# Optimization experiments

Measured on AMD Instinct MI355X. Metric: run time of the kernel, lower is better.

The kernel has to match this reference:

```python
import jax, jax.numpy as jnp
import numpy as np

NEG_INF = -9e15  # mask value used by the original module
LEAKY_SLOPE = 0.2


def setup_inputs() -> dict:
    key = jax.random.key(0)
    k1, k2, k3, k4 = jax.random.split(key, 4)
    B, N, F_in = 4, 2048, 128
    H, head_dim = 4, 32
    h = jax.random.normal(k1, (B, N, F_in), dtype=jnp.float32)
    adj = jax.random.randint(k2, (N, N), 0, 2, dtype=jnp.int32)
    W = jax.random.normal(k3, (H, F_in, head_dim), dtype=jnp.float32)
    a = jax.random.normal(k4, (H, 2 * head_dim, 1), dtype=jnp.float32)
    return {"h": h, "adj": adj, "W": W, "a": a}


def reference(h, adj, W, a):
    # h: (B, N, F_in); adj: (N, N) int; W: (H, F_in, D); a: (H, 2D, 1)
    D = W.shape[-1]
    Wh = jnp.einsum('bnf,hfd->bhnd', h, W)          # (B, H, N, D)
    # Original builds [Wh_i || Wh_j] @ a. Split a so that
    # e_ij = Wh_i . a_src + Wh_j . a_dst  (identical math, no N^2*2D concat).
    a_src = a[:, :D, 0]                              # (H, D)
    a_dst = a[:, D:, 0]                              # (H, D)
    e_src = jnp.einsum('bhnd,hd->bhn', Wh, a_src)    # (B, H, N)
    e_dst = jnp.einsum('bhnd,hd->bhn', Wh, a_dst)    # (B, H, N)
    e = jax.nn.leaky_relu(e_src[..., :, None] + e_dst[..., None, :],
                          negative_slope=LEAKY_SLOPE)  # (B, H, N, N)
    masked = jnp.where(adj[None, None] > 0, e, NEG_INF)
    attn = jax.nn.softmax(masked, axis=-1)           # dropout: eval mode (identity)
    out = jnp.einsum('bhij,bhjd->bhid', attn, Wh)    # (B, H, N, D)
    B, H, N, _ = out.shape
    # concat heads along feature dim == transpose to (B, N, H, D) then merge
    return out.transpose(0, 2, 1, 3).reshape(B, N, H * D)
```

## Files before the change

kernel.cpp:

```cpp
#include <hip/hip_runtime.h>
#include <hip/hip_bf16.h>

typedef unsigned short u16;
using f32x4 = __attribute__((ext_vector_type(4))) float;
using short8 = __attribute__((ext_vector_type(8))) short;

constexpr int B_ = 4, N_ = 2048, FIN = 128, H_ = 4, D_ = 32;
constexpr int BH = B_ * H_;
constexpr float LOG2E = 1.4426950408889634f;

constexpr int NPB = 16;

__global__ __launch_bounds__(256) void wh_kernel(
    const float* __restrict__ h, const float* __restrict__ W,
    const float* __restrict__ a, u16* __restrict__ WhT,
    float* __restrict__ es, float* __restrict__ ed) {
  __shared__ float hsh[NPB][FIN];
  __shared__ float part[NPB][H_][D_];
  const int t = threadIdx.x;
  const int fh = t >> 7, hh = (t >> 5) & 3, d = t & 31;

  float Wr[64];
#pragma unroll
  for (int ff = 0; ff < 64; ++ff)
    Wr[ff] = W[hh * (FIN * D_) + (fh * 64 + ff) * D_ + d];

  const int n0 = blockIdx.x * NPB;
  for (int idx = t; idx < NPB * FIN; idx += 256)
    hsh[idx >> 7][idx & 127] = h[(size_t)n0 * FIN + idx];
  __syncthreads();

  float accs[NPB];
#pragma unroll
  for (int r = 0; r < NPB; ++r) {
    float acc = 0.f;
    const float* hr = &hsh[r][fh * 64];
#pragma unroll
    for (int f4 = 0; f4 < 16; ++f4) {
      float4 hv = *(const float4*)(hr + f4 * 4);
      acc += hv.x * Wr[f4 * 4 + 0];
      acc += hv.y * Wr[f4 * 4 + 1];
      acc += hv.z * Wr[f4 * 4 + 2];
      acc += hv.w * Wr[f4 * 4 + 3];
    }
    accs[r] = acc;
  }
  if (fh == 0) {
#pragma unroll
    for (int r = 0; r < NPB; ++r) part[r][hh][d] = accs[r];
  }
  __syncthreads();
  if (fh == 1) {
    const int b = n0 / N_;
    const int bh = b * H_ + hh;
    const int n0r = n0 & (N_ - 1);
    const float asrc = a[hh * 2 * D_ + d];
    const float adst = a[hh * 2 * D_ + D_ + d];
    union { u16 s[16]; uint4 q[2]; } wbuf;
#pragma unroll
    for (int r = 0; r < NPB; ++r) {
      const float wh = accs[r] + part[r][hh][d];
      union { __hip_bfloat16 h; u16 u; } cv;
      cv.h = __float2bfloat16(wh);
      wbuf.s[r] = cv.u;
      float vs = wh * asrc, vd = wh * adst;
#pragma unroll
      for (int o = 16; o >= 1; o >>= 1) {
        vs += __shfl_xor(vs, o, 64);
        vd += __shfl_xor(vd, o, 64);
      }
      if (d == 0) {
        es[(size_t)bh * N_ + n0r + r] = vs * LOG2E;
        ed[(size_t)bh * N_ + n0r + r] = vd * LOG2E;
      }
    }
    u16* dst = WhT + ((size_t)(bh * 32 + d)) * N_ + n0r;
    *(uint4*)dst = wbuf.q[0];
    *(uint4*)(dst + 8) = wbuf.q[1];
  }
}

__global__ __launch_bounds__(256) void pack_kernel(
    const int* __restrict__ adj, unsigned long long* __restrict__ mask) {
  const int gid = blockIdx.x * 256 + threadIdx.x;
  const int wdx = gid >> 6;
  const int lane = threadIdx.x & 63;
  const int i = wdx >> 5;
  const int jb = (wdx & 31) << 6;
  const int v = adj[(size_t)i * N_ + jb + lane];
  const unsigned long long m = __ballot(v > 0);
  if (lane == 0) mask[wdx] = m;
}

constexpr int ROWS = 16;
constexpr int NSTEP = 16;

__global__ __launch_bounds__(256, 6) void attn_kernel(
    const float* __restrict__ es, const float* __restrict__ ed,
    const u16* __restrict__ WhT, const unsigned int* __restrict__ mask32,
    float* __restrict__ out) {
  __shared__ __align__(16) char arena[12352];
  __shared__ float essh[ROWS], rmsh[ROWS];
  __shared__ float sumsh[4][16];

  float* edsh = (float*)arena;
  unsigned int* maskw = (unsigned int*)(arena + 8192);
  unsigned char* maskb = (unsigned char*)(arena + 8192);

  const int bh = blockIdx.x >> 7;
  const int i0 = (blockIdx.x & 127) * ROWS;
  const int tid = threadIdx.x, lane = tid & 63, w = tid >> 6;
  const int jq = w;

  const float* edb = ed + (size_t)bh * N_;
  *(float4*)&edsh[tid * 8] = *(const float4*)(edb + tid * 8);
  *(float4*)&edsh[tid * 8 + 4] = *(const float4*)(edb + tid * 8 + 4);
  const unsigned int* mrow = mask32 + (size_t)i0 * 64;
#pragma unroll
  for (int q = 0; q < 4; ++q) {
    const int idx = tid + q * 256;
    maskw[(idx >> 6) * 65 + (idx & 63)] = mrow[(idx >> 6) * 64 + (idx & 63)];
  }
  if (tid < ROWS) essh[tid] = es[(size_t)bh * N_ + i0 + tid];
  __syncthreads();

#pragma unroll
  for (int q4 = 0; q4 < 4; ++q4) {
    const int r = w * 4 + q4;
    float mx = -3.0e38f;
#pragma unroll
    for (int q = 0; q < 32; ++q) {
      const unsigned int mword = maskw[r * 65 + q * 2 + (lane >> 5)];
      const float v = edsh[q * 64 + lane];
      mx = ((mword >> (lane & 31)) & 1u) ? fmaxf(mx, v) : mx;
    }
#pragma unroll
    for (int o = 32; o >= 1; o >>= 1) mx = fmaxf(mx, __shfl_xor(mx, o, 64));
    if (lane == 0) rmsh[r] = mx;
  }
  __syncthreads();

  const int row16 = lane & 15, kg = lane >> 4;
  const float esr = essh[row16];
  const float xm = esr + rmsh[row16];
  const float mxr = fmaxf(xm, 0.2f * xm);
  const float cpos = esr - mxr;
  const float cneg = 0.2f * esr - mxr;
  const float thr = -esr;

  const u16* wb0 = WhT + ((size_t)(bh * 32 + row16)) * N_ + jq * 512 + kg * 8;
  const u16* wb1 = wb0 + (size_t)16 * N_;

  short8 ones;
#pragma unroll
  for (int q = 0; q < 8; ++q) ones[q] = (short)0x3F80;

  f32x4 c0 = {}, c1 = {}, csum = {};
  short8 b0 = *(const short8*)wb0;
  short8 b1 = *(const short8*)wb1;

  for (int s = 0; s < NSTEP; ++s) {
    const int sn = (s + 1 < NSTEP) ? (s + 1) : (NSTEP - 1);
    const short8 nb0 = *(const short8*)(wb0 + sn * 32);
    const short8 nb1 = *(const short8*)(wb1 + sn * 32);

    const int k0 = jq * 512 + s * 32;
    const unsigned int mb = maskb[row16 * 260 + (k0 >> 3) + kg];
    const float4 ea = *(const float4*)&edsh[k0 + kg * 8];
    const float4 eb = *(const float4*)&edsh[k0 + kg * 8 + 4];
    const float ev[8] = {ea.x, ea.y, ea.z, ea.w, eb.x, eb.y, eb.z, eb.w};
    float p[8];
#pragma unroll
    for (int j = 0; j < 8; ++j) {
      const float edv = ev[j];
      const float zp = edv + cpos;
      const float zn = __builtin_fmaf(edv, 0.2f, cneg);
      float z = (edv >= thr) ? zp : zn;
      z = (mb & (1u << j)) ? z : -1e30f;
      p[j] = exp2f(z);
    }
    union { unsigned int u[4]; short8 v8; } af;
    asm("v_cvt_pk_bf16_f32 %0, %1, %2" : "=v"(af.u[0]) : "v"(p[0]), "v"(p[1]));
    asm("v_cvt_pk_bf16_f32 %0, %1, %2" : "=v"(af.u[1]) : "v"(p[2]), "v"(p[3]));
    asm("v_cvt_pk_bf16_f32 %0, %1, %2" : "=v"(af.u[2]) : "v"(p[4]), "v"(p[5]));
    asm("v_cvt_pk_bf16_f32 %0, %1, %2" : "=v"(af.u[3]) : "v"(p[6]), "v"(p[7]));

    c0 = __builtin_amdgcn_mfma_f32_16x16x32_bf16(af.v8, b0, c0, 0, 0, 0);
    c1 = __builtin_amdgcn_mfma_f32_16x16x32_bf16(af.v8, b1, c1, 0, 0, 0);
    csum = __builtin_amdgcn_mfma_f32_16x16x32_bf16(af.v8, ones, csum, 0, 0, 0);
    b0 = nb0;
    b1 = nb1;
  }

  __syncthreads();

  float* redc = (float*)arena;
#pragma unroll
  for (int r = 0; r < 4; ++r) {
    redc[(jq * 16 + kg * 4 + r) * 33 + row16] = c0[r];
    redc[(jq * 16 + kg * 4 + r) * 33 + 16 + row16] = c1[r];
  }
  if (row16 == 0) {
#pragma unroll
    for (int r = 0; r < 4; ++r) sumsh[jq][kg * 4 + r] = csum[r];
  }
  __syncthreads();

  if (tid < 128) {
    const int r = tid >> 3;
    const int c4 = (tid & 7) * 4;
    const float inv =
        1.f / fmaxf(sumsh[0][r] + sumsh[1][r] + sumsh[2][r] + sumsh[3][r],
                    1e-30f);
    float4 o;
    const float* p0 = &redc[(0 * 16 + r) * 33 + c4];
    const float* p1 = &redc[(1 * 16 + r) * 33 + c4];
    const float* p2 = &redc[(2 * 16 + r) * 33 + c4];
    const float* p3 = &redc[(3 * 16 + r) * 33 + c4];
    o.x = (p0[0] + p1[0] + p2[0] + p3[0]) * inv;
    o.y = (p0[1] + p1[1] + p2[1] + p3[1]) * inv;
    o.z = (p0[2] + p1[2] + p2[2] + p3[2]) * inv;
    o.w = (p0[3] + p1[3] + p2[3] + p3[3]) * inv;
    const int b = bh >> 2, hh = bh & 3;
    *(float4*)&out[((size_t)(b * N_ + i0 + r)) * (H_ * D_) + hh * 32 + c4] = o;
  }
}

extern "C" void kernel_launch(void* const* d_in, const int* in_sizes, int n_in,
                              void* d_out, int out_size, void* d_ws,
                              size_t ws_size, hipStream_t stream) {
  const float* h = (const float*)d_in[0];
  const int* adj = (const int*)d_in[1];
  const float* W = (const float*)d_in[2];
  const float* a = (const float*)d_in[3];
  char* ws = (char*)d_ws;
  u16* WhT = (u16*)ws;
  float* es = (float*)(ws + (2u << 20));
  float* ed = (float*)(ws + (2u << 20) + (128u << 10));
  unsigned long long* mask =
      (unsigned long long*)(ws + (2u << 20) + (256u << 10));
  float* out = (float*)d_out;

  wh_kernel<<<B_ * N_ / NPB, 256, 0, stream>>>(h, W, a, WhT, es, ed);
  pack_kernel<<<N_ * N_ / 256, 256, 0, stream>>>(adj, mask);
  attn_kernel<<<BH * (N_ / ROWS), 256, 0, stream>>>(
      es, ed, WhT, (const unsigned int*)mask, out);
}
```

Baseline: 133.8 us.

## Streamline attention inner loop with bit-select masking and raise occupancy target

```diff
diff --git a/kernel.cpp b/kernel.cpp
--- a/kernel.cpp
+++ b/kernel.cpp
@@ -8,6 +8,10 @@
 constexpr int B_ = 4, N_ = 2048, FIN = 128, H_ = 4, D_ = 32;
 constexpr int BH = B_ * H_;
 constexpr float LOG2E = 1.4426950408889634f;
+
+static __device__ __forceinline__ float bitsel(int m, float a, unsigned int bu) {
+  return __uint_as_float((__float_as_uint(a) & (unsigned)m) | (bu & ~(unsigned)m));
+}
 
 constexpr int NPB = 16;
 
@@ -95,7 +99,7 @@
 constexpr int ROWS = 16;
 constexpr int NSTEP = 16;
 
-__global__ __launch_bounds__(256, 6) void attn_kernel(
+__global__ __launch_bounds__(256, 8) void attn_kernel(
     const float* __restrict__ es, const float* __restrict__ ed,
     const u16* __restrict__ WhT, const unsigned int* __restrict__ mask32,
     float* __restrict__ out) {
@@ -105,7 +109,6 @@
 
   float* edsh = (float*)arena;
   unsigned int* maskw = (unsigned int*)(arena + 8192);
-  unsigned char* maskb = (unsigned char*)(arena + 8192);
 
   const int bh = blockIdx.x >> 7;
   const int i0 = (blockIdx.x & 127) * ROWS;
@@ -124,19 +127,36 @@
   if (tid < ROWS) essh[tid] = es[(size_t)bh * N_ + i0 + tid];
   __syncthreads();
 
-#pragma unroll
-  for (int q4 = 0; q4 < 4; ++q4) {
-    const int r = w * 4 + q4;
-    float mx = -3.0e38f;
-#pragma unroll
+  {
+    const unsigned int NEGU = __float_as_uint(-3.0e38f);
+    float mx0 = -3.0e38f, mx1 = -3.0e38f, mx2 = -3.0e38f, mx3 = -3.0e38f;
+    const int l31 = lane & 31, lh = lane >> 5;
+#pragma unroll 8
     for (int q = 0; q < 32; ++q) {
-      const unsigned int mword = maskw[r * 65 + q * 2 + (lane >> 5)];
-      const float v = edsh[q * 64 + lane];
-      mx = ((mword >> (lane & 31)) & 1u) ? fmaxf(mx, v) : mx;
-    }
-#pragma unroll
-    for (int o = 32; o >= 1; o >>= 1) mx = fmaxf(mx, __shfl_xor(mx, o, 64));
-    if (lane == 0) rmsh[r] = mx;
+      const float edv = edsh[q * 64 + lane];
+      const int base = w * 4 * 65 + q * 2 + lh;
+      const int b0 = __builtin_amdgcn_sbfe((int)maskw[base], l31, 1);
+      const int b1 = __builtin_amdgcn_sbfe((int)maskw[base + 65], l31, 1);
+      const int b2 = __builtin_amdgcn_sbfe((int)maskw[base + 130], l31, 1);
+      const int b3 = __builtin_amdgcn_sbfe((int)maskw[base + 195], l31, 1);
+      mx0 = fmaxf(mx0, bitsel(b0, edv, NEGU));
+      mx1 = fmaxf(mx1, bitsel(b1, edv, NEGU));
+      mx2 = fmaxf(mx2, bitsel(b2, edv, NEGU));
+      mx3 = fmaxf(mx3, bitsel(b3, edv, NEGU));
+    }
+#pragma unroll
+    for (int o = 32; o >= 1; o >>= 1) {
+      mx0 = fmaxf(mx0, __shfl_xor(mx0, o, 64));
+      mx1 = fmaxf(mx1, __shfl_xor(mx1, o, 64));
+      mx2 = fmaxf(mx2, __shfl_xor(mx2, o, 64));
+      mx3 = fmaxf(mx3, __shfl_xor(mx3, o, 64));
+    }
+    if (lane == 0) {
+      rmsh[w * 4 + 0] = mx0;
+      rmsh[w * 4 + 1] = mx1;
+      rmsh[w * 4 + 2] = mx2;
+      rmsh[w * 4 + 3] = mx3;
+    }
   }
   __syncthreads();
 
@@ -146,28 +166,28 @@
   const float mxr = fmaxf(xm, 0.2f * xm);
   const float cpos = esr - mxr;
   const float cneg = 0.2f * esr - mxr;
-  const float thr = -esr;
+  const unsigned int NEGZ = __float_as_uint(-1.0e30f);
 
   const u16* wb0 = WhT + ((size_t)(bh * 32 + row16)) * N_ + jq * 512 + kg * 8;
   const u16* wb1 = wb0 + (size_t)16 * N_;
+  const unsigned int* mwp = maskw + row16 * 65 + jq * 16;
+  const float* edq = edsh + jq * 512 + kg * 8;
+  const int kg8 = kg << 3;
 
   short8 ones;
 #pragma unroll
   for (int q = 0; q < 8; ++q) ones[q] = (short)0x3F80;
 
   f32x4 c0 = {}, c1 = {}, csum = {};
-  short8 b0 = *(const short8*)wb0;
-  short8 b1 = *(const short8*)wb1;
-
+
+#pragma unroll 4
   for (int s = 0; s < NSTEP; ++s) {
-    const int sn = (s + 1 < NSTEP) ? (s + 1) : (NSTEP - 1);
-    const short8 nb0 = *(const short8*)(wb0 + sn * 32);
-    const short8 nb1 = *(const short8*)(wb1 + sn * 32);
-
-    const int k0 = jq * 512 + s * 32;
-    const unsigned int mb = maskb[row16 * 260 + (k0 >> 3) + kg];
-    const float4 ea = *(const float4*)&edsh[k0 + kg * 8];
-    const float4 eb = *(const float4*)&edsh[k0 + kg * 8 + 4];
+    const short8 b0 = *(const short8*)(wb0 + s * 32);
+    const short8 b1 = *(const short8*)(wb1 + s * 32);
+
+    const unsigned int mw = mwp[s] >> kg8;
+    const float4 ea = *(const float4*)(edq + s * 32);
+    const float4 eb = *(const float4*)(edq + s * 32 + 4);
     const float ev[8] = {ea.x, ea.y, ea.z, ea.w, eb.x, eb.y, eb.z, eb.w};
     float p[8];
 #pragma unroll
@@ -175,9 +195,9 @@
       const float edv = ev[j];
       const float zp = edv + cpos;
       const float zn = __builtin_fmaf(edv, 0.2f, cneg);
-      float z = (edv >= thr) ? zp : zn;
-      z = (mb & (1u << j)) ? z : -1e30f;
-      p[j] = exp2f(z);
+      const float z = fmaxf(zp, zn);
+      const int mbit = __builtin_amdgcn_sbfe((int)mw, j, 1);
+      p[j] = __builtin_amdgcn_exp2f(bitsel(mbit, z, NEGZ));
     }
     union { unsigned int u[4]; short8 v8; } af;
     asm("v_cvt_pk_bf16_f32 %0, %1, %2" : "=v"(af.u[0]) : "v"(p[0]), "v"(p[1]));
@@ -188,8 +208,6 @@
     c0 = __builtin_amdgcn_mfma_f32_16x16x32_bf16(af.v8, b0, c0, 0, 0, 0);
     c1 = __builtin_amdgcn_mfma_f32_16x16x32_bf16(af.v8, b1, c1, 0, 0, 0);
     csum = __builtin_amdgcn_mfma_f32_16x16x32_bf16(af.v8, ones, csum, 0, 0, 0);
-    b0 = nb0;
-    b1 = nb1;
   }
 
   __syncthreads();
```

After: 125.5 us. 1.07x faster.
